# Performance work log

Hardware: AMD Instinct MI355X
Metric: run time of the kernel (lower is better)

The kernel has to match this reference:

```python
import jax, jax.numpy as jnp
import numpy as np

N = 4096; E = 65536; IN = 512; H = 256; QD = 256; NH = 8; HD = QD // NH
OUT = 10; L = 2; CT = 50


def _ln(x, g, b, eps=1e-5):
    mu = x.mean(-1, keepdims=True)
    var = ((x - mu) ** 2).mean(-1, keepdims=True)
    return (x - mu) * jax.lax.rsqrt(var + eps) * g + b


def _forward(x, edge_index, cell_types, Wi, bi, Wq, bq, Wk, bk, Wv, bv, Bc, cemb,
             Win, bin_p, Wo, bo, Wm1, bm1, Wm2, bm2, Wm3, bm3, ln_g, ln_b,
             Wc1, bc1, Wc2, bc2):
    src, tgt = edge_index[0], edge_index[1]
    h = jax.nn.relu(x @ Wi + bi)                      # [N, H] input projection
    # graph connectivity scattered into a dense mask (as in _create_attention_mask)
    mask = jnp.zeros((N, N), jnp.float32).at[src, tgt].set(1.0)
    for l in range(L):
        res = h
        Q = h @ Wq[l] + bq[l]                         # [N, QD]
        K = h @ Wk[l] + bk[l]
        V = h @ Wv[l] + bv[l]
        Q = Q @ Bc[l]                                 # biological constraint
        K = K @ Bc[l].T
        ce = cemb[l][cell_types]                      # [N, QD] cell-type embedding
        Q = Q + 0.1 * ce
        K = K + 0.1 * ce
        # dense graph-masked attention (entanglement matrix), applied to V
        scores = (Q @ K.T) / float(np.sqrt(QD))      # [N, N]
        scores = jnp.where(mask == 0.0, -1e9, scores)
        attn = jax.nn.softmax(scores, axis=-1)
        graph_att = attn @ V                          # [N, QD]
        # nn.MultiheadAttention(Q, K, V) entanglement layer (eval mode)
        q = (Q @ Win[l, :, :QD] + bin_p[l, :QD]).reshape(N, NH, HD)
        k = (K @ Win[l, :, QD:2 * QD] + bin_p[l, QD:2 * QD]).reshape(N, NH, HD)
        v = (V @ Win[l, :, 2 * QD:] + bin_p[l, 2 * QD:]).reshape(N, NH, HD)
        w = jax.nn.softmax(jnp.einsum('nhd,mhd->hnm', q, k) / float(np.sqrt(HD)), axis=-1)
        mha = jnp.einsum('hnm,mhd->nhd', w, v).reshape(N, QD) @ Wo[l] + bo[l]
        # edge gather -> message MLP -> scatter-add (PyG aggr='add', x_i=target, x_j=source)
        # quantum slot of the concat is zeros, so only the first 2H rows of Wm1 contribute
        m = jnp.concatenate([h[tgt], h[src]], axis=-1) @ Wm1[l, :2 * H] + bm1[l]
        m = jax.nn.relu(m)
        m = jax.nn.relu(m @ Wm2[l] + bm2[l])
        m = m @ Wm3[l] + bm3[l]                       # [E, H]
        agg = jax.ops.segment_sum(m, tgt, num_segments=N)
        h = _ln(res + agg + mha + graph_att, ln_g[l], ln_b[l])
    # graph-level readout: mean || max pooling -> classifier (hidden*2 -> hidden -> out)
    pooled = jnp.concatenate([h.mean(0), h.max(0)], axis=-1)   # [2H]
    z = jax.nn.relu(pooled @ Wc1 + bc1)
    return z @ Wc2 + bc2                              # [OUT]


def setup_inputs():
    ks = jax.random.split(jax.random.key(0), 40)
    s = 0.05
    p = lambda i, shape: jax.random.normal(ks[i], shape, jnp.float32) * s
    z = lambda shape: jnp.zeros(shape, jnp.float32)
    return {
        'x': jax.random.normal(ks[0], (N, IN), jnp.float32),
        'edge_index': jax.random.randint(ks[1], (2, E), 0, N),
        'cell_types': jax.random.randint(ks[2], (N,), 0, CT),
        'Wi': p(3, (IN, H)), 'bi': z((H,)),
        'Wq': p(4, (L, H, QD)), 'bq': z((L, QD)),
        'Wk': p(5, (L, H, QD)), 'bk': z((L, QD)),
        'Wv': p(6, (L, H, QD)), 'bv': z((L, QD)),
        'Bc': p(7, (L, QD, QD)),
        'cemb': p(8, (L, CT, QD)),
        'Win': p(9, (L, QD, 3 * QD)), 'bin_p': z((L, 3 * QD)),
        'Wo': p(10, (L, QD, QD)), 'bo': z((L, QD)),
        'Wm1': p(11, (L, 2 * H + QD, QD)), 'bm1': z((L, QD)),
        'Wm2': p(12, (L, QD, QD)), 'bm2': z((L, QD)),
        'Wm3': p(13, (L, QD, H)), 'bm3': z((L, H)),
        'ln_g': jnp.ones((L, H), jnp.float32), 'ln_b': z((L, H)),
        'Wc1': p(14, (2 * H, H)), 'bc1': z((H,)),
        'Wc2': p(15, (H, OUT)), 'bc2': z((OUT,)),
    }


def reference(x, edge_index, cell_types, Wi, bi, Wq, bq, Wk, bk, Wv, bv, Bc, cemb,
              Win, bin_p, Wo, bo, Wm1, bm1, Wm2, bm2, Wm3, bm3, ln_g, ln_b,
              Wc1, bc1, Wc2, bc2):
    return _forward(x, edge_index, cell_types, Wi, bi, Wq, bq, Wk, bk, Wv, bv, Bc, cemb,
                    Win, bin_p, Wo, bo, Wm1, bm1, Wm2, bm2, Wm3, bm3, ln_g, ln_b,
                    Wc1, bc1, Wc2, bc2)
```

## Files before the change

### kernel.cpp

```cpp
#include <hip/hip_runtime.h>
#include <hip/hip_bf16.h>

#define N_NODES 4096
#define E_EDGES 65536
#define IN_F    512
#define H_F     256
#define QD      256
#define NHEAD   8
#define HD      32
#define OUT_F   10
#define L_LAYERS 2
#define CT_N    50

enum { FLAG_RELU = 1, FLAG_ACCUM = 2, FLAG_WF32 = 4, FLAG_WB16 = 8 };

typedef __attribute__((ext_vector_type(8))) __bf16 bf16x8;
typedef __attribute__((ext_vector_type(4))) float f32x4;

union PU { bf16x8 v; __hip_bfloat16 h[8]; __hip_bfloat162 b2[4]; };

template<int BM, int BN, bool EDGE>
__global__ __launch_bounds__(256) void gemm_mfma(
    const __hip_bfloat16* __restrict__ A, int lda,
    const __hip_bfloat16* __restrict__ B, int ldb,
    float* __restrict__ Cf, __hip_bfloat16* __restrict__ Cb, int ldc,
    int K,
    const float* __restrict__ bias, const float* __restrict__ rowscale,
    const int* __restrict__ tgtp, const int* __restrict__ srcp,
    const float* __restrict__ kbias,
    int flags)
{
    constexpr int WM = BM / 2, WN = BN / 2, MT = WM / 16, NT = WN / 16;
    constexpr int LDT = 40;
    __shared__ alignas(16) __hip_bfloat16 As[BM * LDT];
    __shared__ alignas(16) __hip_bfloat16 Bs[BN * LDT];

    const int tid = threadIdx.x;
    const int w = tid >> 6, lane = tid & 63, l16 = lane & 15, quad = lane >> 4;
    const int wm = w >> 1, wn = w & 1;
    const int bm = blockIdx.y * BM, bn = blockIdx.x * BN;

    f32x4 acc[MT][NT];
    #pragma unroll
    for (int i = 0; i < MT; ++i)
        #pragma unroll
        for (int j = 0; j < NT; ++j)
            #pragma unroll
            for (int r = 0; r < 4; ++r) acc[i][j][r] = 0.f;

    for (int k0 = 0; k0 < K; k0 += 32) {
        #pragma unroll
        for (int f = tid; f < BM * 4; f += 256) {
            int r = f >> 2, sg = f & 3;
            if (EDGE) {
                int i = bm + r;
                int tg = tgtp[i], sr = srcp[i];
                PU z1, z2, o;
                z1.v = *reinterpret_cast<const bf16x8*>(A + (size_t)tg * 512 + k0 + sg * 8);
                z2.v = *reinterpret_cast<const bf16x8*>(A + (size_t)sr * 512 + 256 + k0 + sg * 8);
                float4 b0 = *reinterpret_cast<const float4*>(kbias + k0 + sg * 8);
                float4 b1 = *reinterpret_cast<const float4*>(kbias + k0 + sg * 8 + 4);
                float bb[8] = {b0.x, b0.y, b0.z, b0.w, b1.x, b1.y, b1.z, b1.w};
                #pragma unroll
                for (int j = 0; j < 8; ++j) {
                    float v = __bfloat162float(z1.h[j]) + __bfloat162float(z2.h[j]) + bb[j];
                    o.h[j] = __float2bfloat16(fmaxf(v, 0.f));
                }
                *reinterpret_cast<bf16x8*>(&As[r * LDT + sg * 8]) = o.v;
            } else {
                *reinterpret_cast<uint4*>(&As[r * LDT + sg * 8]) =
                    *reinterpret_cast<const uint4*>(A + (size_t)(bm + r) * lda + k0 + sg * 8);
            }
        }
        #pragma unroll
        for (int f = tid; f < BN * 4; f += 256) {
            int r = f >> 2, sg = f & 3;
            *reinterpret_cast<uint4*>(&Bs[r * LDT + sg * 8]) =
                *reinterpret_cast<const uint4*>(B + (size_t)(bn + r) * ldb + k0 + sg * 8);
        }
        __syncthreads();
        bf16x8 af[MT], bfr[NT];
        #pragma unroll
        for (int mt = 0; mt < MT; ++mt)
            af[mt] = *reinterpret_cast<const bf16x8*>(&As[(wm * WM + mt * 16 + l16) * LDT + quad * 8]);
        #pragma unroll
        for (int nt = 0; nt < NT; ++nt)
            bfr[nt] = *reinterpret_cast<const bf16x8*>(&Bs[(wn * WN + nt * 16 + l16) * LDT + quad * 8]);
        #pragma unroll
        for (int mt = 0; mt < MT; ++mt)
            #pragma unroll
            for (int nt = 0; nt < NT; ++nt)
                acc[mt][nt] = __builtin_amdgcn_mfma_f32_16x16x32_bf16(af[mt], bfr[nt], acc[mt][nt], 0, 0, 0);
        __syncthreads();
    }

    #pragma unroll
    for (int mt = 0; mt < MT; ++mt) {
        #pragma unroll
        for (int nt = 0; nt < NT; ++nt) {
            int col = bn + wn * WN + nt * 16 + l16;
            #pragma unroll
            for (int r = 0; r < 4; ++r) {
                int row = bm + wm * WM + mt * 16 + quad * 4 + r;
                float v = acc[mt][nt][r];
                if (bias) {
                    float bv = bias[col];
                    if (rowscale) bv *= rowscale[row];
                    v += bv;
                }
                if (flags & FLAG_RELU) v = fmaxf(v, 0.f);
                size_t off = (size_t)row * ldc + col;
                if (flags & FLAG_ACCUM)     Cf[off] += v;
                else if (flags & FLAG_WF32) Cf[off] = v;
                if (flags & FLAG_WB16)      Cb[off] = __float2bfloat16(v);
            }
        }
    }
}

__global__ __launch_bounds__(512) void edge_gemm(
    const __hip_bfloat16* __restrict__ Z,
    const __hip_bfloat16* __restrict__ B,
    __hip_bfloat16* __restrict__ C,
    const int* __restrict__ tgtp, const int* __restrict__ srcp,
    const float* __restrict__ kbias,
    const float* __restrict__ bias)
{
    constexpr int LDA = 264;
    constexpr int LDB = 40;
    __shared__ alignas(16) __hip_bfloat16 As[64 * LDA];
    __shared__ alignas(16) __hip_bfloat16 Bs[256 * LDB];

    const int tid = threadIdx.x;
    const int w = tid >> 6, lane = tid & 63, l16 = lane & 15, quad = lane >> 4;
    const int bid = blockIdx.x;
    const int bm = ((bid & 7) * 128 + (bid >> 3)) * 64;

    bf16x8 zt[4], zs[4];
    #pragma unroll
    for (int u = 0; u < 4; ++u) {
        int g = u * 512 + tid;
        int r = g >> 5, c = g & 31;
        int i = bm + r;
        int tg = tgtp[i], sr = srcp[i];
        zt[u] = *reinterpret_cast<const bf16x8*>(Z + (size_t)tg * 512 + c * 8);
        zs[u] = *reinterpret_cast<const bf16x8*>(Z + (size_t)sr * 512 + 256 + c * 8);
    }
    #pragma unroll
    for (int u = 0; u < 4; ++u) {
        int g = u * 512 + tid;
        int r = g >> 5, c = g & 31;
        PU a, b, o;
        a.v = zt[u]; b.v = zs[u];
        float4 k0v = *reinterpret_cast<const float4*>(kbias + c * 8);
        float4 k1v = *reinterpret_cast<const float4*>(kbias + c * 8 + 4);
        float bb[8] = {k0v.x, k0v.y, k0v.z, k0v.w, k1v.x, k1v.y, k1v.z, k1v.w};
        #pragma unroll
        for (int j = 0; j < 8; ++j) {
            float v = __bfloat162float(a.h[j]) + __bfloat162float(b.h[j]) + bb[j];
            o.h[j] = __float2bfloat16(fmaxf(v, 0.f));
        }
        *reinterpret_cast<bf16x8*>(&As[r * LDA + c * 8]) = o.v;
    }

    const int wn = w;
    f32x4 acc[4][2];
    #pragma unroll
    for (int mt = 0; mt < 4; ++mt)
        #pragma unroll
        for (int nt = 0; nt < 2; ++nt)
            #pragma unroll
            for (int r = 0; r < 4; ++r) acc[mt][nt][r] = 0.f;

    for (int k0 = 0; k0 < 256; k0 += 32) {
        #pragma unroll
        for (int u = 0; u < 2; ++u) {
            int f = u * 512 + tid;
            int r = f >> 2, sg = f & 3;
            *reinterpret_cast<uint4*>(&Bs[r * LDB + sg * 8]) =
                *reinterpret_cast<const uint4*>(B + (size_t)r * 256 + k0 + sg * 8);
        }
        __syncthreads();
        bf16x8 af[4], bfr[2];
        #pragma unroll
        for (int mt = 0; mt < 4; ++mt)
            af[mt] = *reinterpret_cast<const bf16x8*>(&As[(mt * 16 + l16) * LDA + k0 + quad * 8]);
        #pragma unroll
        for (int nt = 0; nt < 2; ++nt)
            bfr[nt] = *reinterpret_cast<const bf16x8*>(&Bs[(wn * 32 + nt * 16 + l16) * LDB + quad * 8]);
        #pragma unroll
        for (int mt = 0; mt < 4; ++mt)
            #pragma unroll
            for (int nt = 0; nt < 2; ++nt)
                acc[mt][nt] = __builtin_amdgcn_mfma_f32_16x16x32_bf16(af[mt], bfr[nt], acc[mt][nt], 0, 0, 0);
        __syncthreads();
    }

    #pragma unroll
    for (int mt = 0; mt < 4; ++mt) {
        #pragma unroll
        for (int nt = 0; nt < 2; ++nt) {
            int col = wn * 32 + nt * 16 + l16;
            float bv = bias[col];
            #pragma unroll
            for (int r = 0; r < 4; ++r) {
                int row = bm + mt * 16 + quad * 4 + r;
                float v = fmaxf(acc[mt][nt][r] + bv, 0.f);
                C[(size_t)row * 256 + col] = __float2bfloat16(v);
            }
        }
    }
}

struct GSet { const __hip_bfloat16* A; int lda; const __hip_bfloat16* B;
              const float* bias; const float* rowscale;
              const float* extra; float esc; float cscale;
              __hip_bfloat16* C; float* Cf; int vtout; int ldc; int coloff; };
struct GPack { GSet s[8]; };

__global__ __launch_bounds__(256) void gemm_bz(GPack p, const int* __restrict__ eidx)
{
    GSet g = p.s[blockIdx.z];
    constexpr int LDT = 40;
    __shared__ alignas(16) __hip_bfloat16 As[64 * LDT];
    __shared__ alignas(16) __hip_bfloat16 Bs[64 * LDT];

    const int tid = threadIdx.x;
    const int w = tid >> 6, lane = tid & 63, l16 = lane & 15, quad = lane >> 4;
    const int wm = w >> 1, wn = w & 1;
    const int bm = blockIdx.y * 64, bn = blockIdx.x * 64;

    f32x4 acc[2][2];
    #pragma unroll
    for (int i = 0; i < 2; ++i)
        #pragma unroll
        for (int j = 0; j < 2; ++j)
            #pragma unroll
            for (int r = 0; r < 4; ++r) acc[i][j][r] = 0.f;

    for (int k0 = 0; k0 < 256; k0 += 32) {
        #pragma unroll
        for (int f = tid; f < 256; f += 256) {
            int r = f >> 2, sg = f & 3;
            *reinterpret_cast<uint4*>(&As[r * LDT + sg * 8]) =
                *reinterpret_cast<const uint4*>(g.A + (size_t)(bm + r) * g.lda + k0 + sg * 8);
            *reinterpret_cast<uint4*>(&Bs[r * LDT + sg * 8]) =
                *reinterpret_cast<const uint4*>(g.B + (size_t)(bn + r) * 256 + k0 + sg * 8);
        }
        __syncthreads();
        bf16x8 af[2], bfr[2];
        #pragma unroll
        for (int mt = 0; mt < 2; ++mt)
            af[mt] = *reinterpret_cast<const bf16x8*>(&As[(wm * 32 + mt * 16 + l16) * LDT + quad * 8]);
        #pragma unroll
        for (int nt = 0; nt < 2; ++nt)
            bfr[nt] = *reinterpret_cast<const bf16x8*>(&Bs[(wn * 32 + nt * 16 + l16) * LDT + quad * 8]);
        #pragma unroll
        for (int mt = 0; mt < 2; ++mt)
            #pragma unroll
            for (int nt = 0; nt < 2; ++nt)
                acc[mt][nt] = __builtin_amdgcn_mfma_f32_16x16x32_bf16(af[mt], bfr[nt], acc[mt][nt], 0, 0, 0);
        __syncthreads();
    }

    #pragma unroll
    for (int mt = 0; mt < 2; ++mt) {
        #pragma unroll
        for (int nt = 0; nt < 2; ++nt) {
            int colL = bn + wn * 32 + nt * 16 + l16;
            #pragma unroll
            for (int r = 0; r < 4; ++r) {
                int row = bm + wm * 32 + mt * 16 + quad * 4 + r;
                float v = acc[mt][nt][r];
                if (g.bias) {
                    float bv = g.bias[colL];
                    if (g.rowscale) bv *= g.rowscale[row];
                    v += bv;
                }
                if (g.extra) v += g.esc * g.extra[(size_t)eidx[row] * QD + colL];
                v *= g.cscale;
                if (g.vtout)
                    g.C[(size_t)colL * 4096 + row] = __float2bfloat16(v);
                else if (g.Cf)
                    g.Cf[(size_t)row * g.ldc + g.coloff + colL] = v;
                else
                    g.C[(size_t)row * g.ldc + g.coloff + colL] = __float2bfloat16(v);
            }
        }
    }
}

struct FDesc { const float* A; int lda; const float* B; int ldb; int tb;
               const float* bias; float* C; int M, N, K; };
struct FPack { FDesc d[16]; };

__global__ __launch_bounds__(256) void fgemm2(FPack p)
{
    FDesc c = p.d[blockIdx.z];
    int bm = blockIdx.y * 32, bn = blockIdx.x * 32;
    if (bm >= c.M || bn >= c.N) return;
    __shared__ float As[16][33];
    __shared__ float Bs[16][33];
    int tid = threadIdx.x;
    int tr = tid / 16, tc = tid % 16;
    float acc[2][2] = {};

    for (int k0 = 0; k0 < c.K; k0 += 16) {
        #pragma unroll
        for (int u = 0; u < 2; ++u) {
            int i = tid * 2 + u;
            int m = i >> 4, kk = i & 15;
            int row = bm + m, kg = k0 + kk;
            As[kk][m] = (row < c.M && kg < c.K) ? c.A[(size_t)row * c.lda + kg] : 0.f;
        }
        if (c.tb) {
            #pragma unroll
            for (int u = 0; u < 2; ++u) {
                int i = tid * 2 + u;
                int n = i >> 4, kk = i & 15;
                int col = bn + n, kg = k0 + kk;
                Bs[kk][n] = (col < c.N && kg < c.K) ? c.B[(size_t)col * c.ldb + kg] : 0.f;
            }
        } else {
            #pragma unroll
            for (int u = 0; u < 2; ++u) {
                int i = tid * 2 + u;
                int kk = i >> 5, n = i & 31;
                int col = bn + n, kg = k0 + kk;
                Bs[kk][n] = (col < c.N && kg < c.K) ? c.B[(size_t)kg * c.ldb + col] : 0.f;
            }
        }
        __syncthreads();
        #pragma unroll
        for (int kk = 0; kk < 16; ++kk) {
            float a0 = As[kk][tr * 2], a1 = As[kk][tr * 2 + 1];
            float b0 = Bs[kk][tc * 2], b1 = Bs[kk][tc * 2 + 1];
            acc[0][0] = fmaf(a0, b0, acc[0][0]);
            acc[0][1] = fmaf(a0, b1, acc[0][1]);
            acc[1][0] = fmaf(a1, b0, acc[1][0]);
            acc[1][1] = fmaf(a1, b1, acc[1][1]);
        }
        __syncthreads();
    }

    #pragma unroll
    for (int i = 0; i < 2; ++i) {
        int row = bm + tr * 2 + i;
        if (row >= c.M) continue;
        #pragma unroll
        for (int j = 0; j < 2; ++j) {
            int col = bn + tc * 2 + j;
            if (col >= c.N) continue;
            float v = acc[i][j];
            if (c.bias) v += c.bias[col];
            c.C[(size_t)row * c.N + col] = v;
        }
    }
}

__global__ __launch_bounds__(512) void mha_flash9(
    const __hip_bfloat16* __restrict__ Qm,
    const __hip_bfloat16* __restrict__ Km,
    const __hip_bfloat16* __restrict__ Vt, __hip_bfloat16* __restrict__ Out)
{
    const int hh = blockIdx.y;
    const int tid = threadIdx.x;
    const int w = tid >> 6, lane = tid & 63, l16 = lane & 15, quad = lane >> 4;
    const int qb = blockIdx.x * 32;

    __shared__ float Osh[7][2][64][8];
    __shared__ float Lsh[7][2][16];

    const bf16x8 aq0 = *reinterpret_cast<const bf16x8*>(
        Qm + (size_t)(qb + l16) * 256 + hh * 32 + quad * 8);
    const bf16x8 aq1 = *reinterpret_cast<const bf16x8*>(
        Qm + (size_t)(qb + 16 + l16) * 256 + hh * 32 + quad * 8);
    const __hip_bfloat16* vb0 = Vt + (size_t)(hh * 32 + l16) * 4096;
    const __hip_bfloat16* vb1 = vb0 + (size_t)16 * 4096;
    const int rowoff = (l16 >> 2) * 8 + (l16 & 3);
    const f32x4 zero = {0.f, 0.f, 0.f, 0.f};

    f32x4 o00 = zero, o01 = zero, o10 = zero, o11 = zero;
    float l0 = 0.f, l1 = 0.f;

    const int kstart = w * 512;
    for (int kt = 0; kt < 8; ++kt) {
        const int kbase = kstart + kt * 64;
        bf16x8 kf[4];
        #pragma unroll
        for (int c = 0; c < 2; ++c)
            #pragma unroll
            for (int st = 0; st < 2; ++st)
                kf[c * 2 + st] = *reinterpret_cast<const bf16x8*>(
                    Km + (size_t)(kbase + c * 32 + st * 4 + rowoff) * 256 + hh * 32 + quad * 8);
        bf16x8 v00 = *reinterpret_cast<const bf16x8*>(vb0 + kbase + quad * 8);
        bf16x8 v01 = *reinterpret_cast<const bf16x8*>(vb1 + kbase + quad * 8);
        bf16x8 v10 = *reinterpret_cast<const bf16x8*>(vb0 + kbase + 32 + quad * 8);
        bf16x8 v11 = *reinterpret_cast<const bf16x8*>(vb1 + kbase + 32 + quad * 8);

        {
            f32x4 s[4];
            #pragma unroll
            for (int i = 0; i < 4; ++i)
                s[i] = __builtin_amdgcn_mfma_f32_16x16x32_bf16(kf[i], aq0, zero, 0, 0, 0);
            PU p0, p1;
            float ls = 0.f;
            #pragma unroll
            for (int i = 0; i < 4; ++i) {
                float e0 = exp2f(s[i][0]), e1 = exp2f(s[i][1]);
                float e2 = exp2f(s[i][2]), e3 = exp2f(s[i][3]);
                ls += (e0 + e1) + (e2 + e3);
                PU& pp = (i < 2) ? p0 : p1;
                pp.b2[(i & 1) * 2 + 0] = __float22bfloat162_rn(make_float2(e0, e1));
                pp.b2[(i & 1) * 2 + 1] = __float22bfloat162_rn(make_float2(e2, e3));
            }
            l0 += ls;
            o00 = __builtin_amdgcn_mfma_f32_16x16x32_bf16(v00, p0.v, o00, 0, 0, 0);
            o01 = __builtin_amdgcn_mfma_f32_16x16x32_bf16(v01, p0.v, o01, 0, 0, 0);
            o00 = __builtin_amdgcn_mfma_f32_16x16x32_bf16(v10, p1.v, o00, 0, 0, 0);
            o01 = __builtin_amdgcn_mfma_f32_16x16x32_bf16(v11, p1.v, o01, 0, 0, 0);
        }
        {
            f32x4 s[4];
            #pragma unroll
            for (int i = 0; i < 4; ++i)
                s[i] = __builtin_amdgcn_mfma_f32_16x16x32_bf16(kf[i], aq1, zero, 0, 0, 0);
            PU p0, p1;
            float ls = 0.f;
            #pragma unroll
            for (int i = 0; i < 4; ++i) {
                float e0 = exp2f(s[i][0]), e1 = exp2f(s[i][1]);
                float e2 = exp2f(s[i][2]), e3 = exp2f(s[i][3]);
                ls += (e0 + e1) + (e2 + e3);
                PU& pp = (i < 2) ? p0 : p1;
                pp.b2[(i & 1) * 2 + 0] = __float22bfloat162_rn(make_float2(e0, e1));
                pp.b2[(i & 1) * 2 + 1] = __float22bfloat162_rn(make_float2(e2, e3));
            }
            l1 += ls;
            o10 = __builtin_amdgcn_mfma_f32_16x16x32_bf16(v00, p0.v, o10, 0, 0, 0);
            o11 = __builtin_amdgcn_mfma_f32_16x16x32_bf16(v01, p0.v, o11, 0, 0, 0);
            o10 = __builtin_amdgcn_mfma_f32_16x16x32_bf16(v10, p1.v, o10, 0, 0, 0);
            o11 = __builtin_amdgcn_mfma_f32_16x16x32_bf16(v11, p1.v, o11, 0, 0, 0);
        }
    }

    l0 += __shfl_xor(l0, 16); l0 += __shfl_xor(l0, 32);
    l1 += __shfl_xor(l1, 16); l1 += __shfl_xor(l1, 32);

    if (w > 0) {
        #pragma unroll
        for (int r = 0; r < 4; ++r) {
            Osh[w - 1][0][lane][r]     = o00[r];
            Osh[w - 1][0][lane][4 + r] = o01[r];
            Osh[w - 1][1][lane][r]     = o10[r];
            Osh[w - 1][1][lane][4 + r] = o11[r];
        }
        if (quad == 0) { Lsh[w - 1][0][l16] = l0; Lsh[w - 1][1][l16] = l1; }
    }
    __syncthreads();
    if (w == 0) {
        #pragma unroll
        for (int ww = 0; ww < 7; ++ww) {
            #pragma unroll
            for (int r = 0; r < 4; ++r) {
                o00[r] += Osh[ww][0][lane][r];
                o01[r] += Osh[ww][0][lane][4 + r];
                o10[r] += Osh[ww][1][lane][r];
                o11[r] += Osh[ww][1][lane][4 + r];
            }
            l0 += Lsh[ww][0][l16];
            l1 += Lsh[ww][1][l16];
        }
        {
            float inv = 1.f / l0;
            __hip_bfloat16* dst = Out + (size_t)(qb + l16) * 256 + hh * 32;
            #pragma unroll
            for (int r = 0; r < 4; ++r) {
                dst[quad * 4 + r]      = __float2bfloat16(o00[r] * inv);
                dst[16 + quad * 4 + r] = __float2bfloat16(o01[r] * inv);
            }
        }
        {
            float inv = 1.f / l1;
            __hip_bfloat16* dst = Out + (size_t)(qb + 16 + l16) * 256 + hh * 32;
            #pragma unroll
            for (int r = 0; r < 4; ++r) {
                dst[quad * 4 + r]      = __float2bfloat16(o10[r] * inv);
                dst[16 + quad * 4 + r] = __float2bfloat16(o11[r] * inv);
            }
        }
    }
}

__global__ __launch_bounds__(256) void build_mask(const int* __restrict__ src,
                                                  const int* __restrict__ tgt,
                                                  unsigned* __restrict__ mb,
                                                  int* __restrict__ cnt)
{
    int e = blockIdx.x * 256 + threadIdx.x;
    if (e >= E_EDGES) return;
    int t = tgt[e];
    atomicOr(mb + (size_t)src[e] * (N_NODES / 32) + (t >> 5), 1u << (t & 31));
    atomicAdd(&cnt[t], 1);
}

__global__ __launch_bounds__(1024) void csr_scan(const int* __restrict__ cnt, int* __restrict__ off,
                                                 int* __restrict__ cursor, float* __restrict__ degf)
{
    __shared__ int sh[1024];
    int t = threadIdx.x;
    int base = t * 4;
    int c0 = cnt[base], c1 = cnt[base + 1], c2 = cnt[base + 2], c3 = cnt[base + 3];
    int sum = c0 + c1 + c2 + c3;
    sh[t] = sum; __syncthreads();
    for (int d = 1; d < 1024; d <<= 1) {
        int v = (t >= d) ? sh[t - d] : 0;
        __syncthreads();
        sh[t] += v;
        __syncthreads();
    }
    int excl = sh[t] - sum;
    int o0 = excl, o1 = excl + c0, o2 = o1 + c1, o3 = o2 + c2;
    off[base] = o0; off[base + 1] = o1; off[base + 2] = o2; off[base + 3] = o3;
    cursor[base] = o0; cursor[base + 1] = o1; cursor[base + 2] = o2; cursor[base + 3] = o3;
    degf[base] = (float)c0; degf[base + 1] = (float)c1;
    degf[base + 2] = (float)c2; degf[base + 3] = (float)c3;
    if (t == 1023) off[4096] = sh[t];
}

__global__ __launch_bounds__(256) void csr_fill(const int* __restrict__ src, const int* __restrict__ tgt,
                                                int* __restrict__ cursor,
                                                int* __restrict__ srcp, int* __restrict__ tgtp)
{
    int e = blockIdx.x * 256 + threadIdx.x;
    if (e >= E_EDGES) return;
    int t = tgt[e];
    int pos = atomicAdd(&cursor[t], 1);
    srcp[pos] = src[e];
    tgtp[pos] = t;
}

__global__ __launch_bounds__(256) void seg_sum(const int* __restrict__ off,
                                               const __hip_bfloat16* __restrict__ M2,
                                               __hip_bfloat16* __restrict__ A3)
{
    int n = blockIdx.x, t = threadIdx.x;
    int b0 = off[n], b1 = off[n + 1];
    float s = 0.f;
    for (int i = b0; i < b1; ++i)
        s += __bfloat162float(M2[(size_t)i * 256 + t]);
    A3[(size_t)n * 256 + t] = __float2bfloat16(s);
}

__global__ __launch_bounds__(256) void sparse_attn(
    const __hip_bfloat16* __restrict__ Q, const __hip_bfloat16* __restrict__ K,
    const __hip_bfloat16* __restrict__ V, int vld,
    const unsigned* __restrict__ maskb, float* __restrict__ outb)
{
    int i = blockIdx.x, t = threadIdx.x;
    __shared__ float qsh[256];
    __shared__ int   nb[1024];
    __shared__ float sc[1024];
    __shared__ int   cnt;
    __shared__ float red[4];
    __shared__ float smax, ssum;
    if (t == 0) cnt = 0;
    qsh[t] = __bfloat162float(Q[(size_t)i * 256 + t]);
    __syncthreads();
    if (t < 128) {
        unsigned wv = maskb[(size_t)i * 128 + t];
        while (wv) {
            int b = __ffs(wv) - 1; wv &= wv - 1;
            int p = atomicAdd(&cnt, 1);
            nb[p] = t * 32 + b;
        }
    }
    __syncthreads();
    int deg = cnt;
    int wid = t >> 6, lane = t & 63;
    if (deg > 0) {
        for (int n = wid; n < deg; n += 4) {
            union { uint2 u; __hip_bfloat16 h[4]; } kv;
            kv.u = *reinterpret_cast<const uint2*>(K + (size_t)nb[n] * 256 + lane * 4);
            float s = qsh[lane*4+0] * __bfloat162float(kv.h[0]) + qsh[lane*4+1] * __bfloat162float(kv.h[1])
                    + qsh[lane*4+2] * __bfloat162float(kv.h[2]) + qsh[lane*4+3] * __bfloat162float(kv.h[3]);
            #pragma unroll
            for (int off = 32; off; off >>= 1) s += __shfl_xor(s, off);
            if (lane == 0) sc[n] = s * 0.0625f;
        }
        __syncthreads();
        float m = -3.4e38f;
        for (int n = t; n < deg; n += 256) m = fmaxf(m, sc[n]);
        #pragma unroll
        for (int off = 32; off; off >>= 1) m = fmaxf(m, __shfl_xor(m, off));
        if (lane == 0) red[wid] = m;
        __syncthreads();
        if (t == 0) smax = fmaxf(fmaxf(red[0], red[1]), fmaxf(red[2], red[3]));
        __syncthreads();
        float ls = 0.f;
        for (int n = t; n < deg; n += 256) { float e = __expf(sc[n] - smax); sc[n] = e; ls += e; }
        #pragma unroll
        for (int off = 32; off; off >>= 1) ls += __shfl_xor(ls, off);
        if (lane == 0) red[wid] = ls;
        __syncthreads();
        if (t == 0) ssum = red[0] + red[1] + red[2] + red[3];
        __syncthreads();
        float inv = 1.f / ssum;
        float o = 0.f;
        for (int n = 0; n < deg; ++n)
            o += sc[n] * __bfloat162float(V[(size_t)nb[n] * vld + t]);
        outb[(size_t)i * 256 + t] = o * inv;
    } else {
        float o = 0.f;
        for (int j = 0; j < N_NODES; ++j) o += __bfloat162float(V[(size_t)j * vld + t]);
        outb[(size_t)i * 256 + t] = o * (1.f / N_NODES);
    }
}

__global__ __launch_bounds__(256) void ln_kernel(float* __restrict__ h, __hip_bfloat16* __restrict__ h16,
                                                 const float* __restrict__ a1,
                                                 const float* __restrict__ a2,
                                                 const float* __restrict__ a3,
                                                 const float* __restrict__ g, const float* __restrict__ b)
{
    int row = blockIdx.x, t = threadIdx.x;
    __shared__ float red[256];
    size_t off = ((size_t)row << 8) + t;
    float v = h[off] + a1[off] + a2[off] + a3[off];
    red[t] = v; __syncthreads();
    for (int s = 128; s > 0; s >>= 1) { if (t < s) red[t] += red[t + s]; __syncthreads(); }
    float mu = red[0] * (1.f / 256.f); __syncthreads();
    float d = v - mu;
    red[t] = d * d; __syncthreads();
    for (int s = 128; s > 0; s >>= 1) { if (t < s) red[t] += red[t + s]; __syncthreads(); }
    float var = red[0] * (1.f / 256.f);
    float r = d * rsqrtf(var + 1e-5f) * g[t] + b[t];
    h[off] = r;
    h16[off] = __float2bfloat16(r);
}

__global__ __launch_bounds__(256) void colpool(const float* __restrict__ h, float* __restrict__ p)
{
    int c = blockIdx.x, t = threadIdx.x;
    __shared__ float rs[256], rm[256];
    float s = 0.f, m = -3.4e38f;
    for (int row = t; row < N_NODES; row += 256) {
        float v = h[((size_t)row << 8) + c];
        s += v; m = fmaxf(m, v);
    }
    rs[t] = s; rm[t] = m; __syncthreads();
    for (int st = 128; st > 0; st >>= 1) {
        if (t < st) { rs[t] += rs[t + st]; rm[t] = fmaxf(rm[t], rm[t + st]); }
        __syncthreads();
    }
    if (t == 0) { p[c] = rs[0] * (1.f / N_NODES); p[256 + c] = rm[0]; }
}

__global__ __launch_bounds__(256) void classifier(const float* __restrict__ pooled,
                                                  const float* __restrict__ Wc1, const float* __restrict__ bc1,
                                                  const float* __restrict__ Wc2, const float* __restrict__ bc2,
                                                  float* __restrict__ out)
{
    __shared__ float p[512];
    __shared__ float z[256];
    int t = threadIdx.x;
    p[t] = pooled[t]; p[256 + t] = pooled[256 + t];
    __syncthreads();
    float s = bc1[t];
    for (int k = 0; k < 512; ++k) s = fmaf(p[k], Wc1[k * 256 + t], s);
    z[t] = fmaxf(s, 0.f);
    __syncthreads();
    if (t < OUT_F) {
        float o = bc2[t];
        for (int j = 0; j < 256; ++j) o = fmaf(z[j], Wc2[j * OUT_F + t], o);
        out[t] = o;
    }
}

struct CDesc { const float* s; __hip_bfloat16* d; int total; };
struct CPack { CDesc d[2]; };
__global__ __launch_bounds__(256) void convert_copy(CPack p)
{
    CDesc c = p.d[blockIdx.y];
    for (int i = blockIdx.x * 256 + threadIdx.x; i < c.total; i += gridDim.x * 256)
        c.d[i] = __float2bfloat16(c.s[i]);
}
struct TDesc { const float* s; __hip_bfloat16* d; int K, N, sld; };
struct TPack { TDesc d[23]; };
__global__ __launch_bounds__(256) void convert_t32(TPack p)
{
    TDesc c = p.d[blockIdx.z];
    int k0 = blockIdx.x * 32, n0 = blockIdx.y * 32;
    if (k0 >= c.K || n0 >= c.N) return;
    __shared__ float t[32][33];
    int tr = threadIdx.x >> 5, tc = threadIdx.x & 31;
    #pragma unroll
    for (int rr = 0; rr < 32; rr += 8)
        t[tc][tr + rr] = c.s[(size_t)(k0 + tr + rr) * c.sld + n0 + tc];
    __syncthreads();
    #pragma unroll
    for (int rr = 0; rr < 32; rr += 8)
        c.d[(size_t)(n0 + tr + rr) * c.K + k0 + tc] = __float2bfloat16(t[tr + rr][tc]);
}

extern "C" void kernel_launch(void* const* d_in, const int* in_sizes, int n_in,
                              void* d_out, int out_size, void* d_ws, size_t ws_size,
                              hipStream_t stream)
{
    const float* x    = (const float*)d_in[0];
    const int*   ei   = (const int*)d_in[1];
    const int*   ct   = (const int*)d_in[2];
    const float* Wi   = (const float*)d_in[3];
    const float* bi   = (const float*)d_in[4];
    const float* Wq   = (const float*)d_in[5];
    const float* bq   = (const float*)d_in[6];
    const float* Wk   = (const float*)d_in[7];
    const float* bk   = (const float*)d_in[8];
    const float* Wv   = (const float*)d_in[9];
    const float* bv   = (const float*)d_in[10];
    const float* Bc   = (const float*)d_in[11];
    const float* cemb = (const float*)d_in[12];
    const float* Win  = (const float*)d_in[13];
    const float* binp = (const float*)d_in[14];
    const float* Wo   = (const float*)d_in[15];
    const float* bo   = (const float*)d_in[16];
    const float* Wm1  = (const float*)d_in[17];
    const float* bm1  = (const float*)d_in[18];
    const float* Wm2  = (const float*)d_in[19];
    const float* bm2  = (const float*)d_in[20];
    const float* Wm3  = (const float*)d_in[21];
    const float* bm3  = (const float*)d_in[22];
    const float* lng  = (const float*)d_in[23];
    const float* lnb  = (const float*)d_in[24];
    const float* Wc1  = (const float*)d_in[25];
    const float* bc1  = (const float*)d_in[26];
    const float* Wc2  = (const float*)d_in[27];
    const float* bc2  = (const float*)d_in[28];

    const int* src = ei;
    const int* tgt = ei + E_EDGES;

    char* wp = (char*)d_ws;
    auto alloc = [&](size_t bytes) { char* r = wp; wp += (bytes + 255) & ~(size_t)255; return r; };
    const size_t NH = (size_t)N_NODES * 256;
    float* h      = (float*)alloc(NH * 4);
    float* a1     = (float*)alloc(NH * 4);
    float* a2     = (float*)alloc(NH * 4);
    float* a3     = (float*)alloc(NH * 4);
    float* pooled = (float*)alloc(512 * 4);
    float* degf   = (float*)alloc(N_NODES * 4);
    __hip_bfloat16* x16 = (__hip_bfloat16*)alloc((size_t)N_NODES * 512 * 2);
    __hip_bfloat16* h16 = (__hip_bfloat16*)alloc(NH * 2);
    __hip_bfloat16* Qb  = (__hip_bfloat16*)alloc(NH * 2);
    __hip_bfloat16* Kb  = (__hip_bfloat16*)alloc(NH * 2);
    __hip_bfloat16* Vb  = (__hip_bfloat16*)alloc(NH * 2);
    __hip_bfloat16* Tq  = (__hip_bfloat16*)alloc(NH * 2);
    __hip_bfloat16* Tk  = (__hip_bfloat16*)alloc(NH * 2);
    __hip_bfloat16* Vt  = (__hip_bfloat16*)alloc(NH * 2);
    __hip_bfloat16* Z12 = (__hip_bfloat16*)alloc((size_t)N_NODES * 512 * 2);
    __hip_bfloat16* M216= (__hip_bfloat16*)alloc((size_t)E_EDGES * 256 * 2);
    __hip_bfloat16* A3  = (__hip_bfloat16*)alloc(NH * 2);
    __hip_bfloat16* Wi_t= (__hip_bfloat16*)alloc((size_t)256 * 512 * 2);
    float *Wqc_f[2], *Wkc_f[2], *Wqm_f[2], *Wkm_f[2], *Wvm_f[2];
    float *bqc[2], *bkc[2], *bqm[2], *bkm[2], *bvm[2], *ceq2[2], *cek2[2];
    for (int l = 0; l < 2; ++l) {
        Wqc_f[l] = (float*)alloc(65536 * 4); Wkc_f[l] = (float*)alloc(65536 * 4);
        Wqm_f[l] = (float*)alloc(65536 * 4); Wkm_f[l] = (float*)alloc(65536 * 4);
        Wvm_f[l] = (float*)alloc(65536 * 4);
        bqc[l] = (float*)alloc(256 * 4); bkc[l] = (float*)alloc(256 * 4);
        bqm[l] = (float*)alloc(256 * 4); bkm[l] = (float*)alloc(256 * 4);
        bvm[l] = (float*)alloc(256 * 4);
        ceq2[l] = (float*)alloc(CT_N * 256 * 4); cek2[l] = (float*)alloc(CT_N * 256 * 4);
    }
    __hip_bfloat16* WB[2][11];
    for (int l = 0; l < 2; ++l)
        for (int m = 0; m < 11; ++m)
            WB[l][m] = (__hip_bfloat16*)alloc(65536 * 2);
    unsigned* maskb = (unsigned*)alloc((size_t)N_NODES * 128 * 4);
    int* cnt    = (int*)alloc(N_NODES * 4);
    int* cursor = (int*)alloc(N_NODES * 4);
    int* off    = (int*)alloc((N_NODES + 1) * 4);
    int* srcp   = (int*)alloc(E_EDGES * 4);
    int* tgtp   = (int*)alloc(E_EDGES * 4);

    CPack cp; cp.d[0] = {x, x16, N_NODES * 512};
    convert_copy<<<dim3(256, 1), 256, 0, stream>>>(cp);

    FPack f1; int n1 = 0;
    FPack f2; int n2 = 0;
    for (int l = 0; l < 2; ++l) {
        const float* Wq_l  = Wq + (size_t)l * 65536;
        const float* Wk_l  = Wk + (size_t)l * 65536;
        const float* Wv_l  = Wv + (size_t)l * 65536;
        const float* Bc_l  = Bc + (size_t)l * 65536;
        const float* Win_l = Win + (size_t)l * 256 * 768;
        const float* ce_l  = cemb + (size_t)l * CT_N * QD;
        const float* bq_l  = bq + l * 256;
        const float* bk_l  = bk + l * 256;
        const float* bv_l  = bv + l * 256;
        const float* bin_l = binp + l * 768;
        f1.d[n1++] = {Wq_l, 256, Bc_l, 256, 0, nullptr, Wqc_f[l], 256, 256, 256};
        f1.d[n1++] = {Wk_l, 256, Bc_l, 256, 1, nullptr, Wkc_f[l], 256, 256, 256};
        f1.d[n1++] = {bq_l, 256, Bc_l, 256, 0, nullptr, bqc[l], 1, 256, 256};
        f1.d[n1++] = {bk_l, 256, Bc_l, 256, 1, nullptr, bkc[l], 1, 256, 256};
        f2.d[n2++] = {Wqc_f[l], 256, Win_l,       768, 0, nullptr, Wqm_f[l], 256, 256, 256};
        f2.d[n2++] = {Wkc_f[l], 256, Win_l + 256, 768, 0, nullptr, Wkm_f[l], 256, 256, 256};
        f2.d[n2++] = {Wv_l,     256, Win_l + 512, 768, 0, nullptr, Wvm_f[l], 256, 256, 256};
        f2.d[n2++] = {ce_l,     256, Win_l,       768, 0, nullptr, ceq2[l], CT_N, 256, 256};
        f2.d[n2++] = {ce_l,     256, Win_l + 256, 768, 0, nullptr, cek2[l], CT_N, 256, 256};
        f2.d[n2++] = {bqc[l],   256, Win_l,       768, 0, bin_l,       bqm[l], 1, 256, 256};
        f2.d[n2++] = {bkc[l],   256, Win_l + 256, 768, 0, bin_l + 256, bkm[l], 1, 256, 256};
        f2.d[n2++] = {bv_l,     256, Win_l + 512, 768, 0, bin_l + 512, bvm[l], 1, 256, 256};
    }
    fgemm2<<<dim3(8, 8, n1), 256, 0, stream>>>(f1);
    fgemm2<<<dim3(8, 8, n2), 256, 0, stream>>>(f2);

    TPack tp; int ndt = 0;
    auto addT = [&](const float* s, __hip_bfloat16* d, int K, int N, int sld) { tp.d[ndt++] = {s, d, K, N, sld}; };
    addT(Wi, Wi_t, 512, 256, 256);
    for (int l = 0; l < 2; ++l) {
        const float* Wv_l  = Wv + (size_t)l * 65536;
        const float* Wo_l  = Wo + (size_t)l * 65536;
        const float* Wm1_l = Wm1 + (size_t)l * (2 * H_F + QD) * QD;
        const float* Wm2_l = Wm2 + (size_t)l * 65536;
        const float* Wm3_l = Wm3 + (size_t)l * 65536;
        addT(Wqc_f[l], WB[l][0], 256, 256, 256);
        addT(Wkc_f[l], WB[l][1], 256, 256, 256);
        addT(Wqm_f[l], WB[l][2], 256, 256, 256);
        addT(Wkm_f[l], WB[l][3], 256, 256, 256);
        addT(Wvm_f[l], WB[l][4], 256, 256, 256);
        addT(Wv_l,     WB[l][5], 256, 256, 256);
        addT(Wo_l,     WB[l][6], 256, 256, 256);
        addT(Wm1_l,             WB[l][7], 256, 256, 256);
        addT(Wm1_l + 256 * 256, WB[l][8], 256, 256, 256);
        addT(Wm2_l,    WB[l][9],  256, 256, 256);
        addT(Wm3_l,    WB[l][10], 256, 256, 256);
    }
    convert_t32<<<dim3(16, 8, ndt), 256, 0, stream>>>(tp);

    hipMemsetAsync(maskb, 0, (size_t)N_NODES * 128 * 4, stream);
    hipMemsetAsync(cnt, 0, N_NODES * 4, stream);
    build_mask<<<E_EDGES / 256, 256, 0, stream>>>(src, tgt, maskb, cnt);
    csr_scan<<<1, 1024, 0, stream>>>(cnt, off, cursor, degf);
    csr_fill<<<E_EDGES / 256, 256, 0, stream>>>(src, tgt, cursor, srcp, tgtp);

    gemm_mfma<64, 64, false><<<dim3(4, 64), 256, 0, stream>>>(
        x16, 512, Wi_t, 512, h, h16, 256, 512,
        bi, nullptr, nullptr, nullptr, nullptr, FLAG_RELU | FLAG_WF32 | FLAG_WB16);

    const float QSCALE = 0.25507693f;

    for (int l = 0; l < L_LAYERS; ++l) {
        const float* ce_l  = cemb + (size_t)l * CT_N * QD;
        const float* bo_l  = bo + l * QD;
        const float* bm1_l = bm1 + l * QD;
        const float* bm2_l = bm2 + l * QD;
        const float* bm3_l = bm3 + l * H_F;
        const float* lng_l = lng + l * H_F;
        const float* lnb_l = lnb + l * H_F;
        const float* bv_l  = bv + l * 256;

        {
            GPack gp;
            gp.s[0] = {h16, 256, WB[l][0], bqc[l], nullptr, ce_l,    0.1f, 1.0f,   Qb,  nullptr, 0, 256, 0};
            gp.s[1] = {h16, 256, WB[l][1], bkc[l], nullptr, ce_l,    0.1f, 1.0f,   Kb,  nullptr, 0, 256, 0};
            gp.s[2] = {h16, 256, WB[l][5], bv_l,   nullptr, nullptr, 0.f,  1.0f,   Vb,  nullptr, 0, 256, 0};
            gp.s[3] = {h16, 256, WB[l][2], bqm[l], nullptr, ceq2[l], 0.1f, QSCALE, Tq,  nullptr, 0, 256, 0};
            gp.s[4] = {h16, 256, WB[l][3], bkm[l], nullptr, cek2[l], 0.1f, 1.0f,   Tk,  nullptr, 0, 256, 0};
            gp.s[5] = {h16, 256, WB[l][4], bvm[l], nullptr, nullptr, 0.f,  1.0f,   Vt,  nullptr, 1, 256, 0};
            gp.s[6] = {h16, 256, WB[l][7], nullptr, nullptr, nullptr, 0.f, 1.0f,   Z12, nullptr, 0, 512, 0};
            gp.s[7] = {h16, 256, WB[l][8], nullptr, nullptr, nullptr, 0.f, 1.0f,   Z12, nullptr, 0, 512, 256};
            gemm_bz<<<dim3(4, 64, 8), 256, 0, stream>>>(gp, ct);
        }

        sparse_attn<<<N_NODES, 256, 0, stream>>>(Qb, Kb, Vb, 256, maskb, a1);

        mha_flash9<<<dim3(128, NHEAD), 512, 0, stream>>>(Tq, Tk, Vt, Qb);

        edge_gemm<<<E_EDGES / 64, 512, 0, stream>>>(
            Z12, WB[l][9], M216, tgtp, srcp, bm1_l, bm2_l);
        seg_sum<<<N_NODES, 256, 0, stream>>>(off, M216, A3);

        {
            GPack gp;
            gp.s[0] = {Qb, 256, WB[l][6],  bo_l,  nullptr, nullptr, 0.f, 1.0f, nullptr, a2, 0, 256, 0};
            gp.s[1] = {A3, 256, WB[l][10], bm3_l, degf,    nullptr, 0.f, 1.0f, nullptr, a3, 0, 256, 0};
            gemm_bz<<<dim3(4, 64, 2), 256, 0, stream>>>(gp, ct);
        }

        ln_kernel<<<N_NODES, 256, 0, stream>>>(h, h16, a1, a2, a3, lng_l, lnb_l);
    }

    colpool<<<H_F, 256, 0, stream>>>(h, pooled);
    classifier<<<1, 256, 0, stream>>>(pooled, Wc1, bc1, Wc2, bc2, (float*)d_out);
}
```

Measured before the change: 551.5 us.

## Process 64 queries per MHA block to reuse K/V fragments, add MFMA priority

The dense multi-head attention kernel now handles 64 query rows per block (four 16-row sub-tiles) instead of 32, so each K and V fragment loaded from global memory feeds twice as many MFMAs, and the grid shrinks to half as many blocks. It wraps MFMA groups in s_setprio to favour matrix issue, pads the shared reduction buffer, and splits the final cross-wave reduction over four waves instead of one. In exchange it holds more accumulator registers per thread and uses more shared memory per block, which with the launch-bounds hint of four waves per SIMD may limit occupancy. It also launches only 512 blocks, which may reduce load balance across the CUs.

New measurement: 515.6 us. 6.5% less time.

```diff
diff --git a/kernel.cpp b/kernel.cpp
--- a/kernel.cpp
+++ b/kernel.cpp
@@ -358,7 +358,7 @@
     }
 }
 
-__global__ __launch_bounds__(512) void mha_flash9(
+__global__ __launch_bounds__(512, 4) void mha_flash10(
     const __hip_bfloat16* __restrict__ Qm,
     const __hip_bfloat16* __restrict__ Km,
     const __hip_bfloat16* __restrict__ Vt, __hip_bfloat16* __restrict__ Out)
@@ -366,22 +366,25 @@
     const int hh = blockIdx.y;
     const int tid = threadIdx.x;
     const int w = tid >> 6, lane = tid & 63, l16 = lane & 15, quad = lane >> 4;
-    const int qb = blockIdx.x * 32;
-
-    __shared__ float Osh[7][2][64][8];
-    __shared__ float Lsh[7][2][16];
-
-    const bf16x8 aq0 = *reinterpret_cast<const bf16x8*>(
-        Qm + (size_t)(qb + l16) * 256 + hh * 32 + quad * 8);
-    const bf16x8 aq1 = *reinterpret_cast<const bf16x8*>(
-        Qm + (size_t)(qb + 16 + l16) * 256 + hh * 32 + quad * 8);
+    const int qb = blockIdx.x * 64;
+
+    __shared__ float Osh[8][4][64][9];
+    __shared__ float Lsh[8][4][16];
+
+    bf16x8 aq[4];
+    #pragma unroll
+    for (int s = 0; s < 4; ++s)
+        aq[s] = *reinterpret_cast<const bf16x8*>(
+            Qm + (size_t)(qb + s * 16 + l16) * 256 + hh * 32 + quad * 8);
     const __hip_bfloat16* vb0 = Vt + (size_t)(hh * 32 + l16) * 4096;
     const __hip_bfloat16* vb1 = vb0 + (size_t)16 * 4096;
     const int rowoff = (l16 >> 2) * 8 + (l16 & 3);
     const f32x4 zero = {0.f, 0.f, 0.f, 0.f};
 
-    f32x4 o00 = zero, o01 = zero, o10 = zero, o11 = zero;
-    float l0 = 0.f, l1 = 0.f;
+    f32x4 o0[4], o1[4];
+    float lsum[4];
+    #pragma unroll
+    for (int s = 0; s < 4; ++s) { o0[s] = zero; o1[s] = zero; lsum[s] = 0.f; }
 
     const int kstart = w * 512;
     for (int kt = 0; kt < 8; ++kt) {
@@ -398,96 +401,70 @@
         bf16x8 v10 = *reinterpret_cast<const bf16x8*>(vb0 + kbase + 32 + quad * 8);
         bf16x8 v11 = *reinterpret_cast<const bf16x8*>(vb1 + kbase + 32 + quad * 8);
 
-        {
-            f32x4 s[4];
+        #pragma unroll
+        for (int s = 0; s < 4; ++s) {
+            f32x4 sv[4];
+            __builtin_amdgcn_s_setprio(1);
             #pragma unroll
             for (int i = 0; i < 4; ++i)
-                s[i] = __builtin_amdgcn_mfma_f32_16x16x32_bf16(kf[i], aq0, zero, 0, 0, 0);
+                sv[i] = __builtin_amdgcn_mfma_f32_16x16x32_bf16(kf[i], aq[s], zero, 0, 0, 0);
+            __builtin_amdgcn_s_setprio(0);
             PU p0, p1;
             float ls = 0.f;
             #pragma unroll
             for (int i = 0; i < 4; ++i) {
-                float e0 = exp2f(s[i][0]), e1 = exp2f(s[i][1]);
-                float e2 = exp2f(s[i][2]), e3 = exp2f(s[i][3]);
+                float e0 = exp2f(sv[i][0]), e1 = exp2f(sv[i][1]);
+                float e2 = exp2f(sv[i][2]), e3 = exp2f(sv[i][3]);
                 ls += (e0 + e1) + (e2 + e3);
                 PU& pp = (i < 2) ? p0 : p1;
                 pp.b2[(i & 1) * 2 + 0] = __float22bfloat162_rn(make_float2(e0, e1));
                 pp.b2[(i & 1) * 2 + 1] = __float22bfloat162_rn(make_float2(e2, e3));
             }
-            l0 += ls;
-            o00 = __builtin_amdgcn_mfma_f32_16x16x32_bf16(v00, p0.v, o00, 0, 0, 0);
-            o01 = __builtin_amdgcn_mfma_f32_16x16x32_bf16(v01, p0.v, o01, 0, 0, 0);
-            o00 = __builtin_amdgcn_mfma_f32_16x16x32_bf16(v10, p1.v, o00, 0, 0, 0);
-            o01 = __builtin_amdgcn_mfma_f32_16x16x32_bf16(v11, p1.v, o01, 0, 0, 0);
-        }
-        {
-            f32x4 s[4];
-            #pragma unroll
-            for (int i = 0; i < 4; ++i)
-                s[i] = __builtin_amdgcn_mfma_f32_16x16x32_bf16(kf[i], aq1, zero, 0, 0, 0);
-            PU p0, p1;
-            float ls = 0.f;
-            #pragma unroll
-            for (int i = 0; i < 4; ++i) {
-                float e0 = exp2f(s[i][0]), e1 = exp2f(s[i][1]);
-                float e2 = exp2f(s[i][2]), e3 = exp2f(s[i][3]);
-                ls += (e0 + e1) + (e2 + e3);
-                PU& pp = (i < 2) ? p0 : p1;
-                pp.b2[(i & 1) * 2 + 0] = __float22bfloat162_rn(make_float2(e0, e1));
-                pp.b2[(i & 1) * 2 + 1] = __float22bfloat162_rn(make_float2(e2, e3));
+            lsum[s] += ls;
+            __builtin_amdgcn_s_setprio(1);
+            o0[s] = __builtin_amdgcn_mfma_f32_16x16x32_bf16(v00, p0.v, o0[s], 0, 0, 0);
+            o1[s] = __builtin_amdgcn_mfma_f32_16x16x32_bf16(v01, p0.v, o1[s], 0, 0, 0);
+            o0[s] = __builtin_amdgcn_mfma_f32_16x16x32_bf16(v10, p1.v, o0[s], 0, 0, 0);
+            o1[s] = __builtin_amdgcn_mfma_f32_16x16x32_bf16(v11, p1.v, o1[s], 0, 0, 0);
+            __builtin_amdgcn_s_setprio(0);
+        }
+    }
+
+    #pragma unroll
+    for (int s = 0; s < 4; ++s) {
+        lsum[s] += __shfl_xor(lsum[s], 16);
+        lsum[s] += __shfl_xor(lsum[s], 32);
+    }
+
+    #pragma unroll
+    for (int s = 0; s < 4; ++s) {
+        #pragma unroll
+        for (int r = 0; r < 4; ++r) {
+            Osh[w][s][lane][r]     = o0[s][r];
+            Osh[w][s][lane][4 + r] = o1[s][r];
+        }
+        if (quad == 0) Lsh[w][s][l16] = lsum[s];
+    }
+    __syncthreads();
+    if (w < 4) {
+        const int s = w;
+        f32x4 a0 = zero, a1 = zero;
+        float ll = 0.f;
+        #pragma unroll
+        for (int ww = 0; ww < 8; ++ww) {
+            #pragma unroll
+            for (int r = 0; r < 4; ++r) {
+                a0[r] += Osh[ww][s][lane][r];
+                a1[r] += Osh[ww][s][lane][4 + r];
             }
-            l1 += ls;
-            o10 = __builtin_amdgcn_mfma_f32_16x16x32_bf16(v00, p0.v, o10, 0, 0, 0);
-            o11 = __builtin_amdgcn_mfma_f32_16x16x32_bf16(v01, p0.v, o11, 0, 0, 0);
-            o10 = __builtin_amdgcn_mfma_f32_16x16x32_bf16(v10, p1.v, o10, 0, 0, 0);
-            o11 = __builtin_amdgcn_mfma_f32_16x16x32_bf16(v11, p1.v, o11, 0, 0, 0);
-        }
-    }
-
-    l0 += __shfl_xor(l0, 16); l0 += __shfl_xor(l0, 32);
-    l1 += __shfl_xor(l1, 16); l1 += __shfl_xor(l1, 32);
-
-    if (w > 0) {
+            ll += Lsh[ww][s][l16];
+        }
+        float inv = 1.f / ll;
+        __hip_bfloat16* dst = Out + (size_t)(qb + s * 16 + l16) * 256 + hh * 32;
         #pragma unroll
         for (int r = 0; r < 4; ++r) {
-            Osh[w - 1][0][lane][r]     = o00[r];
-            Osh[w - 1][0][lane][4 + r] = o01[r];
-            Osh[w - 1][1][lane][r]     = o10[r];
-            Osh[w - 1][1][lane][4 + r] = o11[r];
-        }
-        if (quad == 0) { Lsh[w - 1][0][l16] = l0; Lsh[w - 1][1][l16] = l1; }
-    }
-    __syncthreads();
-    if (w == 0) {
-        #pragma unroll
-        for (int ww = 0; ww < 7; ++ww) {
-            #pragma unroll
-            for (int r = 0; r < 4; ++r) {
-                o00[r] += Osh[ww][0][lane][r];
-                o01[r] += Osh[ww][0][lane][4 + r];
-                o10[r] += Osh[ww][1][lane][r];
-                o11[r] += Osh[ww][1][lane][4 + r];
-            }
-            l0 += Lsh[ww][0][l16];
-            l1 += Lsh[ww][1][l16];
-        }
-        {
-            float inv = 1.f / l0;
-            __hip_bfloat16* dst = Out + (size_t)(qb + l16) * 256 + hh * 32;
-            #pragma unroll
-            for (int r = 0; r < 4; ++r) {
-                dst[quad * 4 + r]      = __float2bfloat16(o00[r] * inv);
-                dst[16 + quad * 4 + r] = __float2bfloat16(o01[r] * inv);
-            }
-        }
-        {
-            float inv = 1.f / l1;
-            __hip_bfloat16* dst = Out + (size_t)(qb + 16 + l16) * 256 + hh * 32;
-            #pragma unroll
-            for (int r = 0; r < 4; ++r) {
-                dst[quad * 4 + r]      = __float2bfloat16(o10[r] * inv);
-                dst[16 + quad * 4 + r] = __float2bfloat16(o11[r] * inv);
-            }
+            dst[quad * 4 + r]      = __float2bfloat16(a0[r] * inv);
+            dst[16 + quad * 4 + r] = __float2bfloat16(a1[r] * inv);
         }
     }
 }
@@ -875,7 +852,7 @@
 
         sparse_attn<<<N_NODES, 256, 0, stream>>>(Qb, Kb, Vb, 256, maskb, a1);
 
-        mha_flash9<<<dim3(128, NHEAD), 512, 0, stream>>>(Tq, Tk, Vt, Qb);
+        mha_flash10<<<dim3(64, NHEAD), 512, 0, stream>>>(Tq, Tk, Vt, Qb);
 
         edge_gemm<<<E_EDGES / 64, 512, 0, stream>>>(
             Z12, WB[l][9], M216, tgtp, srcp, bm1_l, bm2_l);
```
